# Kernel tuning notes

Measured on AMD Instinct MI355X. Metric: run time of the kernel, lower is better.

Reference implementation:

```python
import jax, jax.numpy as jnp
import numpy as np

B, H, W, C = 2, 64, 64, 320
GROUPS, EPS = 16, 1e-3  # keras GroupNormalization defaults (C>16 -> groups=16)


def quick_gelu(x):
    return x * jax.nn.sigmoid(x * 1.702)


def group_norm(x, gamma, beta):
    b, h, w, c = x.shape
    xg = x.reshape(b, h, w, GROUPS, c // GROUPS)
    mean = xg.mean(axis=(1, 2, 4), keepdims=True)
    var = xg.var(axis=(1, 2, 4), keepdims=True)
    xg = (xg - mean) * jax.lax.rsqrt(var + EPS)
    return xg.reshape(b, h, w, c) * gamma + beta


def attention(q_in, kv_in, wq, bq, wk, bk, wv, bv, wp, bp):
    # q_in, kv_in: [B,H,W,C]
    b, h, w, c = q_in.shape
    n = h * w
    scale = jnp.asarray(c, q_in.dtype) ** -0.5
    q = (q_in @ wq + bq).reshape(b, n, c)
    k = (kv_in @ wk + bk).reshape(b, n, c)
    v = (kv_in @ wv + bv).reshape(b, n, c)
    s = jax.nn.softmax(jnp.einsum('bnc,bmc->bnm', q, k) * scale, axis=-1)  # [B,N,N]
    o = jnp.einsum('bnm,bmc->bnc', s, v).reshape(b, h, w, c)
    return o @ wp + bp


def setup_inputs() -> dict:
    key = jax.random.key(0)
    ks = jax.random.split(key, 16)
    d = {
        'x': jax.random.normal(ks[0], (B, H, W, C), jnp.float32),
        'context': jax.random.normal(ks[1], (B, H, W, C), jnp.float32),
    }
    names = ['sa_q_w', 'sa_k_w', 'sa_v_w', 'sa_p_w', 'ca_q_w', 'ca_k_w', 'ca_v_w', 'ca_p_w']
    for i, nm in enumerate(names):
        d[nm] = jax.random.normal(ks[2 + i], (C, C), jnp.float32) * 0.02
        d[nm.replace('_w', '_b')] = jnp.zeros((C,), jnp.float32)
    d['ca_norm_g'] = jnp.ones((C,), jnp.float32)
    d['ca_norm_b'] = jnp.zeros((C,), jnp.float32)
    d['geglu_w'] = jax.random.normal(ks[10], (C, 8 * C), jnp.float32) * 0.02  # Conv2D 1x1 -> dense
    d['geglu_b'] = jnp.zeros((8 * C,), jnp.float32)
    d['dense_w'] = jax.random.normal(ks[11], (4 * C, C), jnp.float32) * 0.02
    d['dense_b'] = jnp.zeros((C,), jnp.float32)
    return d


def reference(x, context, sa_q_w, sa_q_b, sa_k_w, sa_k_b, sa_v_w, sa_v_b, sa_p_w, sa_p_b,
              ca_q_w, ca_q_b, ca_k_w, ca_k_b, ca_v_w, ca_v_b, ca_p_w, ca_p_b,
              ca_norm_g, ca_norm_b, geglu_w, geglu_b, dense_w, dense_b):
    # attn1: self-attention (note: its norm is defined but unused in the original call())
    a1 = x + attention(x, x, sa_q_w, sa_q_b, sa_k_w, sa_k_b, sa_v_w, sa_v_b, sa_p_w, sa_p_b)
    x = a1 + x
    # attn2: cross-attention; norm applied to query input, residual uses normalized input
    xn = group_norm(x, ca_norm_g, ca_norm_b)
    a2 = xn + attention(xn, context, ca_q_w, ca_q_b, ca_k_w, ca_k_b, ca_v_w, ca_v_b, ca_p_w, ca_p_b)
    x = a2 + x
    # GEGLU FFN (1x1 convs == dense over channels)
    xp = x @ geglu_w + geglu_b  # [B,H,W,8C]
    hdim = 4 * x.shape[-1]
    ff = xp[..., :hdim] * quick_gelu(xp[..., hdim:])
    return ff @ dense_w + dense_b + x
```

## Files before the change

### kernel.cpp

```cpp
#include <hip/hip_runtime.h>
#include <math.h>
#include <stdint.h>


typedef unsigned short u16;
typedef __attribute__((ext_vector_type(8))) short bf16x8;
typedef __attribute__((ext_vector_type(8))) unsigned short u16x8;
typedef __attribute__((ext_vector_type(4))) float f32x4;

constexpr int Bb = 2, Cc = 320;
constexpr int Nn = 64 * 64;
constexpr int Mm = Bb * Nn;
constexpr int GROUPS = 16, CG = Cc / GROUPS;
constexpr float EPS = 1e-3f;
constexpr int GN_SPLIT = 8;
constexpr int KVS = 4;
constexpr int KVC = Nn / KVS;
constexpr int KVT = 32;
constexpr float THR = 8.f;

__device__ __forceinline__ u16 f2b(float f) {
  unsigned u = __float_as_uint(f);
  unsigned r = u + 0x7fffu + ((u >> 16) & 1u);
  return (u16)(r >> 16);
}
__device__ __forceinline__ float b2f(u16 h) {
  return __uint_as_float(((unsigned)h) << 16);
}

template <bool F32OUT, bool DUAL>
__global__ __launch_bounds__(256) void gemm_nt(
    const u16* __restrict__ A, int lda, long long aZ,
    const u16* __restrict__ B, int ldb, long long bZ,
    const float* __restrict__ bias,
    const float* __restrict__ R1, float alpha1,
    const float* __restrict__ R2,
    void* __restrict__ Cp, int ldc, long long cZ,
    u16* __restrict__ C2,
    int K, float scale) {
  const int z = blockIdx.z;
  A += (long long)z * aZ;
  B += (long long)z * bZ;
  const long long coffz = (long long)z * cZ;

  __shared__ __align__(16) u16 As[128][40];
  __shared__ __align__(16) u16 Bs[64][40];

  const int tid = threadIdx.x;
  const int bm = blockIdx.y * 128, bn = blockIdx.x * 64;
  const int lane = tid & 63;
  const int wid = tid >> 6;
  const int wm = (wid >> 1) * 64, wn = (wid & 1) * 32;
  const int lr = lane & 15, lk = (lane >> 4) * 8;

  const int sr = tid >> 2;
  const int sk = (tid & 3) * 8;

  f32x4 acc[4][2] = {};

  const u16* Ap0 = A + (size_t)(bm + sr) * lda + sk;
  const u16* Ap1 = A + (size_t)(bm + 64 + sr) * lda + sk;
  const u16* Bp0 = B + (size_t)(bn + sr) * ldb + sk;

  for (int k0 = 0; k0 < K; k0 += 32) {
    *reinterpret_cast<u16x8*>(&As[sr][sk]) =
        *reinterpret_cast<const u16x8*>(Ap0 + k0);
    *reinterpret_cast<u16x8*>(&As[64 + sr][sk]) =
        *reinterpret_cast<const u16x8*>(Ap1 + k0);
    *reinterpret_cast<u16x8*>(&Bs[sr][sk]) =
        *reinterpret_cast<const u16x8*>(Bp0 + k0);
    __syncthreads();

    bf16x8 af[4], bfr[2];
#pragma unroll
    for (int i = 0; i < 4; ++i)
      af[i] = *reinterpret_cast<const bf16x8*>(&As[wm + i * 16 + lr][lk]);
#pragma unroll
    for (int j = 0; j < 2; ++j)
      bfr[j] = *reinterpret_cast<const bf16x8*>(&Bs[wn + j * 16 + lr][lk]);
#pragma unroll
    for (int i = 0; i < 4; ++i)
#pragma unroll
      for (int j = 0; j < 2; ++j)
        acc[i][j] = __builtin_amdgcn_mfma_f32_16x16x32_bf16(af[i], bfr[j],
                                                            acc[i][j], 0, 0, 0);
    __syncthreads();
  }

  float* Cf = (float*)Cp;
  u16* Cb = (u16*)Cp;
#pragma unroll
  for (int i = 0; i < 4; ++i)
#pragma unroll
    for (int j = 0; j < 2; ++j)
#pragma unroll
      for (int r = 0; r < 4; ++r) {
        const int row = bm + wm + i * 16 + (lane >> 4) * 4 + r;
        const int col = bn + wn + j * 16 + lr;
        const long long off = (long long)row * ldc + col + coffz;
        float v = acc[i][j][r] * scale;
        if (bias) v += bias[col];
        if (R1) v += alpha1 * R1[off];
        if (R2) v += R2[off];
        if (F32OUT) Cf[off] = v; else Cb[off] = f2b(v);
        if (DUAL) C2[off] = f2b(v);
      }
}

__global__ __launch_bounds__(256, 2) void flash_k(
    const u16* __restrict__ qb, const u16* __restrict__ kb,
    const u16* __restrict__ vtb, float* __restrict__ pO,
    float* __restrict__ pml, float scale) {
  const int qt = blockIdx.x, s = blockIdx.y, b = blockIdx.z;
  const int tid = threadIdx.x, wave = tid >> 6, lane = tid & 63;
  const int lr = lane & 15, hi = lane >> 4;
  const int qrow = qt * 64 + wave * 16;

  __shared__ __align__(16) u16 Ks[KVT][336];
  __shared__ __align__(16) u16 Vts[Cc][40];
  __shared__ __align__(16) u16 plds[4][16][40];

  bf16x8 qreg[10];
  const long long qbase = ((long long)b * Nn + qrow + lr) * Cc;
#pragma unroll
  for (int ks = 0; ks < 10; ++ks)
    qreg[ks] = *reinterpret_cast<const bf16x8*>(qb + qbase + ks * 32 + hi * 8);

  f32x4 accO[20] = {};
  float m[4] = {-INFINITY, -INFINITY, -INFINITY, -INFINITY};
  float l[4] = {0.f, 0.f, 0.f, 0.f};

  const u16* kbb = kb + (long long)b * Nn * Cc;
  const u16* vtbb = vtb + (long long)b * Cc * Nn;
  const int kv0 = s * KVC;

  const int krow = tid >> 3;
  const int kcb = tid & 7;
  u16x8 kst[5], vst[5];

  auto issue = [&](int t) {
    const int kvb = kv0 + t * KVT;
#pragma unroll
    for (int c = 0; c < 5; ++c)
      kst[c] = *reinterpret_cast<const u16x8*>(
          kbb + (long long)(kvb + krow) * Cc + (kcb + 8 * c) * 8);
#pragma unroll
    for (int c = 0; c < 5; ++c) {
      const int id = tid + 256 * c;
      const int vr = id >> 2, vc = id & 3;
      vst[c] = *reinterpret_cast<const u16x8*>(
          vtbb + (long long)vr * Nn + kvb + vc * 8);
    }
  };

  issue(0);
  constexpr int NT = KVC / KVT;
  for (int t = 0; t < NT; ++t) {
    __syncthreads();
#pragma unroll
    for (int c = 0; c < 5; ++c)
      *reinterpret_cast<u16x8*>(&Ks[krow][(kcb + 8 * c) * 8]) = kst[c];
#pragma unroll
    for (int c = 0; c < 5; ++c) {
      const int id = tid + 256 * c;
      const int vr = id >> 2, vc = id & 3;
      *reinterpret_cast<u16x8*>(&Vts[vr][vc * 8]) = vst[c];
    }
    __syncthreads();

    if (t + 1 < NT) issue(t + 1);

    f32x4 accS[2] = {};
    __builtin_amdgcn_s_setprio(1);
#pragma unroll
    for (int ks = 0; ks < 10; ++ks) {
#pragma unroll
      for (int j = 0; j < 2; ++j) {
        const bf16x8 bv =
            *reinterpret_cast<const bf16x8*>(&Ks[j * 16 + lr][ks * 32 + hi * 8]);
        accS[j] =
            __builtin_amdgcn_mfma_f32_16x16x32_bf16(qreg[ks], bv, accS[j], 0, 0, 0);
      }
    }
    __builtin_amdgcn_s_setprio(0);

#pragma unroll
    for (int j = 0; j < 2; ++j)
#pragma unroll
      for (int r = 0; r < 4; ++r) accS[j][r] *= scale;

    float tm[4];
#pragma unroll
    for (int r = 0; r < 4; ++r) {
      float tv = fmaxf(accS[0][r], accS[1][r]);
#pragma unroll
      for (int off = 1; off < 16; off <<= 1) tv = fmaxf(tv, __shfl_xor(tv, off, 64));
      tm[r] = tv;
    }
    const bool grow = (tm[0] > m[0] + THR) | (tm[1] > m[1] + THR) |
                      (tm[2] > m[2] + THR) | (tm[3] > m[3] + THR);
    if (__any(grow)) {
      float resc[4];
#pragma unroll
      for (int r = 0; r < 4; ++r) {
        const float mn = fmaxf(m[r], tm[r]);
        resc[r] = __expf(m[r] - mn);
        m[r] = mn;
        l[r] *= resc[r];
      }
#pragma unroll
      for (int n = 0; n < 20; ++n)
#pragma unroll
        for (int r = 0; r < 4; ++r) accO[n][r] *= resc[r];
    }
#pragma unroll
    for (int r = 0; r < 4; ++r) {
      float ps = 0.f;
#pragma unroll
      for (int j = 0; j < 2; ++j) {
        const float p = __expf(accS[j][r] - m[r]);
        accS[j][r] = p;
        ps += p;
      }
#pragma unroll
      for (int off = 1; off < 16; off <<= 1) ps += __shfl_xor(ps, off, 64);
      l[r] += ps;
    }

#pragma unroll
    for (int j = 0; j < 2; ++j)
#pragma unroll
      for (int r = 0; r < 4; ++r)
        plds[wave][hi * 4 + r][j * 16 + lr] = f2b(accS[j][r]);

    {
      const bf16x8 pa = *reinterpret_cast<const bf16x8*>(&plds[wave][lr][hi * 8]);
      __builtin_amdgcn_s_setprio(1);
#pragma unroll
      for (int n = 0; n < 20; ++n) {
        const bf16x8 bv =
            *reinterpret_cast<const bf16x8*>(&Vts[n * 16 + lr][hi * 8]);
        accO[n] = __builtin_amdgcn_mfma_f32_16x16x32_bf16(pa, bv, accO[n], 0, 0, 0);
      }
      __builtin_amdgcn_s_setprio(0);
    }
  }

  const long long obase = (((long long)(s * Bb + b)) * Nn + qrow) * Cc;
#pragma unroll
  for (int n = 0; n < 20; ++n)
#pragma unroll
    for (int r = 0; r < 4; ++r)
      pO[obase + (long long)(hi * 4 + r) * Cc + n * 16 + lr] = accO[n][r];
  if (lr == 0) {
#pragma unroll
    for (int r = 0; r < 4; ++r) {
      const long long mlb =
          (((long long)(s * Bb + b)) * Nn + qrow + hi * 4 + r) * 2;
      pml[mlb] = m[r];
      pml[mlb + 1] = l[r];
    }
  }
}

__global__ __launch_bounds__(256) void fcomb(const float* __restrict__ pO,
                                             const float* __restrict__ pml,
                                             u16* __restrict__ ob) {
  const int row = blockIdx.x * 8 + (threadIdx.x >> 5);
  const int lane32 = threadIdx.x & 31;
  const int b = row >> 12, rb = row & 4095;
  float ms[KVS], ls[KVS], mm = -INFINITY;
#pragma unroll
  for (int s = 0; s < KVS; ++s) {
    const long long i = (((long long)(s * Bb + b)) * Nn + rb) * 2;
    ms[s] = pml[i];
    ls[s] = pml[i + 1];
    mm = fmaxf(mm, ms[s]);
  }
  float w[KVS], den = 0.f;
#pragma unroll
  for (int s = 0; s < KVS; ++s) {
    w[s] = __expf(ms[s] - mm);
    den += w[s] * ls[s];
  }
  const float inv = 1.0f / den;
#pragma unroll
  for (int k = 0; k < 3; ++k) {
    const int c = k * 128 + lane32 * 4;
    if (c < Cc) {
      float4 o = {0.f, 0.f, 0.f, 0.f};
#pragma unroll
      for (int s = 0; s < KVS; ++s) {
        const float4 v = *reinterpret_cast<const float4*>(
            pO + (((long long)(s * Bb + b)) * Nn + rb) * Cc + c);
        o.x += w[s] * v.x;
        o.y += w[s] * v.y;
        o.z += w[s] * v.z;
        o.w += w[s] * v.w;
      }
      ushort4 u;
      u.x = f2b(o.x * inv);
      u.y = f2b(o.y * inv);
      u.z = f2b(o.z * inv);
      u.w = f2b(o.w * inv);
      *reinterpret_cast<ushort4*>(ob + (long long)row * Cc + c) = u;
    }
  }
}

__global__ __launch_bounds__(256) void cast_b(const float* __restrict__ in,
                                              u16* __restrict__ out) {
  const size_t i = ((size_t)blockIdx.x * 256 + threadIdx.x) * 4;
  const float4 v = *reinterpret_cast<const float4*>(in + i);
  ushort4 o;
  o.x = f2b(v.x); o.y = f2b(v.y); o.z = f2b(v.z); o.w = f2b(v.w);
  *reinterpret_cast<ushort4*>(out + i) = o;
}

__global__ __launch_bounds__(256) void tran_f2b(const float* __restrict__ in,
                                                u16* __restrict__ out, int R,
                                                int C, long long inZ,
                                                long long outZ) {
  in += (long long)blockIdx.z * inZ;
  out += (long long)blockIdx.z * outZ;
  __shared__ u16 t[32][33];
  const int c0 = blockIdx.x * 32, r0 = blockIdx.y * 32;
  const int tx = threadIdx.x, ty = threadIdx.y;
#pragma unroll
  for (int i = 0; i < 32; i += 8)
    t[ty + i][tx] = f2b(in[(size_t)(r0 + ty + i) * C + c0 + tx]);
  __syncthreads();
#pragma unroll
  for (int i = 0; i < 32; i += 8)
    out[(size_t)(c0 + ty + i) * R + r0 + tx] = t[tx][ty + i];
}

__global__ __launch_bounds__(256) void gn_stats(const float* __restrict__ x,
                                                float* __restrict__ partials) {
  const int s = blockIdx.x % GN_SPLIT;
  const int bg = blockIdx.x / GN_SPLIT;
  const int b = bg / GROUPS, g = bg % GROUPS;
  const int rows = Nn / GN_SPLIT;
  const float* base = x + (size_t)b * Nn * Cc + g * CG;
  float sum = 0.f, sq = 0.f;
  for (int i = threadIdx.x; i < rows * CG; i += 256) {
    const int r = i / CG, c = i % CG;
    const float v = base[(size_t)(s * rows + r) * Cc + c];
    sum += v; sq += v * v;
  }
#pragma unroll
  for (int off = 32; off >= 1; off >>= 1) {
    sum += __shfl_xor(sum, off, 64);
    sq += __shfl_xor(sq, off, 64);
  }
  __shared__ float rs[4], rq[4];
  const int tid = threadIdx.x;
  if ((tid & 63) == 0) { rs[tid >> 6] = sum; rq[tid >> 6] = sq; }
  __syncthreads();
  if (tid == 0) {
    partials[(bg * GN_SPLIT + s) * 2 + 0] = rs[0] + rs[1] + rs[2] + rs[3];
    partials[(bg * GN_SPLIT + s) * 2 + 1] = rq[0] + rq[1] + rq[2] + rq[3];
  }
}

__global__ __launch_bounds__(256) void gn_apply(
    const float* __restrict__ x, const float* __restrict__ partials,
    const float* __restrict__ gamma, const float* __restrict__ beta,
    float* __restrict__ xn, u16* __restrict__ xnb) {
  const size_t idx = (size_t)blockIdx.x * 256 + threadIdx.x;
  const int c = (int)(idx % Cc);
  const size_t row = idx / Cc;
  const int b = (int)(row / Nn);
  const int bg = b * GROUPS + c / CG;
  float sum = 0.f, sq = 0.f;
#pragma unroll
  for (int s = 0; s < GN_SPLIT; ++s) {
    sum += partials[(bg * GN_SPLIT + s) * 2 + 0];
    sq += partials[(bg * GN_SPLIT + s) * 2 + 1];
  }
  const float cnt = (float)Nn * CG;
  const float mean = sum / cnt;
  const float var = sq / cnt - mean * mean;
  const float r = rsqrtf(var + EPS);
  const float v = (x[idx] - mean) * r * gamma[c] + beta[c];
  xn[idx] = v;
  xnb[idx] = f2b(v);
}

__global__ __launch_bounds__(256) void geglu_comb(const u16* __restrict__ g1,
                                                  const u16* __restrict__ g2,
                                                  u16* __restrict__ ff) {
  const size_t i = ((size_t)blockIdx.x * 256 + threadIdx.x) * 4;
  const ushort4 a = *reinterpret_cast<const ushort4*>(g1 + i);
  const ushort4 b = *reinterpret_cast<const ushort4*>(g2 + i);
  ushort4 o;
  float v1, v2;
  v1 = b2f(a.x); v2 = b2f(b.x);
  o.x = f2b(v1 * (v2 / (1.0f + __expf(-1.702f * v2))));
  v1 = b2f(a.y); v2 = b2f(b.y);
  o.y = f2b(v1 * (v2 / (1.0f + __expf(-1.702f * v2))));
  v1 = b2f(a.z); v2 = b2f(b.z);
  o.z = f2b(v1 * (v2 / (1.0f + __expf(-1.702f * v2))));
  v1 = b2f(a.w); v2 = b2f(b.w);
  o.w = f2b(v1 * (v2 / (1.0f + __expf(-1.702f * v2))));
  *reinterpret_cast<ushort4*>(ff + i) = o;
}

extern "C" void kernel_launch(void* const* d_in, const int* in_sizes, int n_in,
                              void* d_out, int out_size, void* d_ws,
                              size_t ws_size, hipStream_t stream) {
  const float* x   = (const float*)d_in[0];
  const float* ctx = (const float*)d_in[1];
  const float* W[8];
  const float* Bv[8];
  for (int i = 0; i < 8; ++i) {
    W[i]  = (const float*)d_in[2 + 2 * i];
    Bv[i] = (const float*)d_in[3 + 2 * i];
  }
  const float* gn_g = (const float*)d_in[18];
  const float* gn_b = (const float*)d_in[19];
  const float* gw   = (const float*)d_in[20];
  const float* gb   = (const float*)d_in[21];
  const float* dw   = (const float*)d_in[22];
  const float* db   = (const float*)d_in[23];
  float* out = (float*)d_out;

  char* base = (char*)d_ws;
  size_t o = 0;
  auto alloc = [&](size_t bytes) {
    void* p = base + o;
    o = (o + bytes + 255) & ~(size_t)255;
    return p;
  };
  u16* wT[8];
  for (int i = 0; i < 8; ++i) wT[i] = (u16*)alloc(320 * 320 * 2);
  u16* gwT  = (u16*)alloc((size_t)2560 * 320 * 2);
  u16* dwT  = (u16*)alloc((size_t)320 * 1280 * 2);
  u16* xb   = (u16*)alloc((size_t)Mm * Cc * 2);
  u16* ctxb = (u16*)alloc((size_t)Mm * Cc * 2);
  float* x2 = (float*)alloc((size_t)Mm * Cc * 4);
  float* xn = (float*)alloc((size_t)Mm * Cc * 4);
  u16* xnb  = (u16*)alloc((size_t)Mm * Cc * 2);
  float* x3 = (float*)alloc((size_t)Mm * Cc * 4);
  u16* x3b  = (u16*)alloc((size_t)Mm * Cc * 2);
  float* stats = (float*)alloc(4096);
  const size_t SCRSZ = (size_t)20971520 + (size_t)KVS * Bb * Nn * Cc * 4 + 1048576;
  char* SCR = (char*)alloc(SCRSZ);
  u16* qb   = (u16*)SCR;
  u16* kb   = (u16*)(SCR + 5242880);
  u16* vtb  = (u16*)(SCR + 10485760);
  u16* ob   = (u16*)(SCR + 15728640);
  char* REST = SCR + 20971520;
  float* vf  = (float*)REST;
  float* pO  = (float*)REST;
  float* pml = (float*)(REST + (size_t)KVS * Bb * Nn * Cc * 4);
  u16* g1b = (u16*)SCR;
  u16* g2b = (u16*)(SCR + 20971520);
  u16* ffb = (u16*)(SCR + 41943040);

  if (base == nullptr || ws_size < o) return;

  const float scale = 1.0f / sqrtf((float)Cc);
  const long long NC = (long long)Nn * Cc;

  auto gemm_b = [&](const u16* A, int lda, long long aZ, const u16* B, int ldb,
                    long long bZ, const float* bias, u16* C, int ldc,
                    long long cZ, int Mr, int Nc, int K, float sc, int nz) {
    dim3 grid(Nc / 64, Mr / 128, nz);
    gemm_nt<false, false><<<grid, 256, 0, stream>>>(
        A, lda, aZ, B, ldb, bZ, bias, nullptr, 0.f, nullptr, C, ldc, cZ,
        nullptr, K, sc);
  };
  auto gemm_f = [&](const u16* A, int lda, const u16* B, int ldb,
                    const float* bias, const float* R1, float a1,
                    const float* R2, float* C, int ldc, int Mr, int Nc, int K) {
    dim3 grid(Nc / 64, Mr / 128, 1);
    gemm_nt<true, false><<<grid, 256, 0, stream>>>(
        A, lda, 0, B, ldb, 0, bias, R1, a1, R2, C, ldc, 0, nullptr, K, 1.f);
  };

  cast_b<<<(Mm * Cc) / 1024, 256, 0, stream>>>(x, xb);
  cast_b<<<(Mm * Cc) / 1024, 256, 0, stream>>>(ctx, ctxb);
  for (int i = 0; i < 8; ++i)
    tran_f2b<<<dim3(10, 10, 1), dim3(32, 8), 0, stream>>>(W[i], wT[i], 320, 320, 0, 0);
  tran_f2b<<<dim3(80, 10, 1), dim3(32, 8), 0, stream>>>(gw, gwT, 320, 2560, 0, 0);
  tran_f2b<<<dim3(10, 40, 1), dim3(32, 8), 0, stream>>>(dw, dwT, 1280, 320, 0, 0);

  auto attention = [&](const u16* qsrc, const u16* kv, int wi) {
    gemm_b(qsrc, Cc, 0, wT[wi + 0], Cc, 0, Bv[wi + 0], qb, Cc, 0, Mm, Cc, Cc, 1.f, 1);
    gemm_b(kv,   Cc, 0, wT[wi + 1], Cc, 0, Bv[wi + 1], kb, Cc, 0, Mm, Cc, Cc, 1.f, 1);
    {
      dim3 grid(Cc / 64, Mm / 128, 1);
      gemm_nt<true, false><<<grid, 256, 0, stream>>>(
          kv, Cc, 0, wT[wi + 2], Cc, 0, Bv[wi + 2], nullptr, 0.f, nullptr, vf,
          Cc, 0, nullptr, Cc, 1.f);
    }
    tran_f2b<<<dim3(Cc / 32, Nn / 32, 2), dim3(32, 8), 0, stream>>>(
        vf, vtb, Nn, Cc, NC, NC);
    flash_k<<<dim3(Nn / 64, KVS, Bb), 256, 0, stream>>>(qb, kb, vtb, pO, pml,
                                                        scale);
    fcomb<<<Mm / 8, 256, 0, stream>>>(pO, pml, ob);
  };

  attention(xb, xb, 0);
  gemm_f(ob, Cc, wT[3], Cc, Bv[3], x, 2.0f, nullptr, x2, Cc, Mm, Cc, Cc);

  gn_stats<<<Bb * GROUPS * GN_SPLIT, 256, 0, stream>>>(x2, stats);
  gn_apply<<<(Mm * Cc) / 256, 256, 0, stream>>>(x2, stats, gn_g, gn_b, xn, xnb);

  attention(xnb, ctxb, 4);
  {
    dim3 grid(Cc / 64, Mm / 128, 1);
    gemm_nt<true, true><<<grid, 256, 0, stream>>>(
        ob, Cc, 0, wT[7], Cc, 0, Bv[7], xn, 1.0f, x2, x3, Cc, 0, x3b, Cc, 1.f);
  }

  gemm_b(x3b, Cc, 0, gwT, Cc, 0, gb, g1b, 1280, 0, Mm, 1280, Cc, 1.f, 1);
  gemm_b(x3b, Cc, 0, gwT + (size_t)1280 * 320, Cc, 0, gb + 1280, g2b, 1280, 0,
         Mm, 1280, Cc, 1.f, 1);
  geglu_comb<<<(int)(((size_t)Mm * 1280) / 1024), 256, 0, stream>>>(g1b, g2b, ffb);
  gemm_f(ffb, 1280, dwT, 1280, db, x3, 1.0f, nullptr, out, Cc, Mm, Cc, 1280);
}
```

Measured before the change: 607.0 us.

## Fuse QKV projections into one GEMM with transposed V epilogue

Concatenates the Q/K/V (and cross-attention K/V) weights into single wide GEMM launches. V columns are written directly in transposed bf16 layout from the GEMM epilogue, which removes the fp32 V buffer and the separate transpose kernel. It also batches the eight weight transposes into one launch and merges the two GEGLU GEMMs into one 2560-wide GEMM. The cost is strided transposed stores with poor coalescing in the epilogue, plus a bias-concatenation kernel.

```diff
diff --git a/kernel.cpp b/kernel.cpp
--- a/kernel.cpp
+++ b/kernel.cpp
@@ -28,7 +28,7 @@
   return __uint_as_float(((unsigned)h) << 16);
 }
 
-template <bool F32OUT, bool DUAL>
+template <bool F32OUT, bool DUAL, bool VTS>
 __global__ __launch_bounds__(256) void gemm_nt(
     const u16* __restrict__ A, int lda, long long aZ,
     const u16* __restrict__ B, int ldb, long long bZ,
@@ -37,6 +37,7 @@
     const float* __restrict__ R2,
     void* __restrict__ Cp, int ldc, long long cZ,
     u16* __restrict__ C2,
+    u16* __restrict__ VT, int vtc0,
     int K, float scale) {
   const int z = blockIdx.z;
   A += (long long)z * aZ;
@@ -92,23 +93,35 @@
 #pragma unroll
   for (int i = 0; i < 4; ++i)
 #pragma unroll
-    for (int j = 0; j < 2; ++j)
-#pragma unroll
-      for (int r = 0; r < 4; ++r) {
-        const int row = bm + wm + i * 16 + (lane >> 4) * 4 + r;
-        const int col = bn + wn + j * 16 + lr;
-        const long long off = (long long)row * ldc + col + coffz;
-        float v = acc[i][j][r] * scale;
-        if (bias) v += bias[col];
-        if (R1) v += alpha1 * R1[off];
-        if (R2) v += R2[off];
-        if (F32OUT) Cf[off] = v; else Cb[off] = f2b(v);
-        if (DUAL) C2[off] = f2b(v);
+    for (int j = 0; j < 2; ++j) {
+      const int col = bn + wn + j * 16 + lr;
+      const int row0 = bm + wm + i * 16 + (lane >> 4) * 4;
+      if (VTS && col >= vtc0) {
+        const int c = col - vtc0;
+        const int bz = row0 >> 12, rb = row0 & 4095;
+        ushort4 u;
+        u.x = f2b(acc[i][j][0] * scale + bias[col]);
+        u.y = f2b(acc[i][j][1] * scale + bias[col]);
+        u.z = f2b(acc[i][j][2] * scale + bias[col]);
+        u.w = f2b(acc[i][j][3] * scale + bias[col]);
+        *reinterpret_cast<ushort4*>(VT + ((long long)bz * Cc + c) * Nn + rb) = u;
+      } else {
+#pragma unroll
+        for (int r = 0; r < 4; ++r) {
+          const long long off = (long long)(row0 + r) * ldc + col + coffz;
+          float v = acc[i][j][r] * scale;
+          if (bias) v += bias[col];
+          if (R1) v += alpha1 * R1[off];
+          if (R2) v += R2[off];
+          if (F32OUT) Cf[off] = v; else Cb[off] = f2b(v);
+          if (DUAL) C2[off] = f2b(v);
+        }
       }
+    }
 }
 
 __global__ __launch_bounds__(256, 2) void flash_k(
-    const u16* __restrict__ qb, const u16* __restrict__ kb,
+    const u16* __restrict__ q, int qlda, const u16* __restrict__ k, int klda,
     const u16* __restrict__ vtb, float* __restrict__ pO,
     float* __restrict__ pml, float scale) {
   const int qt = blockIdx.x, s = blockIdx.y, b = blockIdx.z;
@@ -121,16 +134,16 @@
   __shared__ __align__(16) u16 plds[4][16][40];
 
   bf16x8 qreg[10];
-  const long long qbase = ((long long)b * Nn + qrow + lr) * Cc;
+  const long long qbase = ((long long)b * Nn + qrow + lr) * qlda;
 #pragma unroll
   for (int ks = 0; ks < 10; ++ks)
-    qreg[ks] = *reinterpret_cast<const bf16x8*>(qb + qbase + ks * 32 + hi * 8);
+    qreg[ks] = *reinterpret_cast<const bf16x8*>(q + qbase + ks * 32 + hi * 8);
 
   f32x4 accO[20] = {};
   float m[4] = {-INFINITY, -INFINITY, -INFINITY, -INFINITY};
   float l[4] = {0.f, 0.f, 0.f, 0.f};
 
-  const u16* kbb = kb + (long long)b * Nn * Cc;
+  const u16* kbb = k + (long long)b * Nn * klda;
   const u16* vtbb = vtb + (long long)b * Cc * Nn;
   const int kv0 = s * KVC;
 
@@ -143,7 +156,7 @@
 #pragma unroll
     for (int c = 0; c < 5; ++c)
       kst[c] = *reinterpret_cast<const u16x8*>(
-          kbb + (long long)(kvb + krow) * Cc + (kcb + 8 * c) * 8);
+          kbb + (long long)(kvb + krow) * klda + (kcb + 8 * c) * 8);
 #pragma unroll
     for (int c = 0; c < 5; ++c) {
       const int id = tid + 256 * c;
@@ -285,8 +298,8 @@
   }
   const float inv = 1.0f / den;
 #pragma unroll
-  for (int k = 0; k < 3; ++k) {
-    const int c = k * 128 + lane32 * 4;
+  for (int kk = 0; kk < 3; ++kk) {
+    const int c = kk * 128 + lane32 * 4;
     if (c < Cc) {
       float4 o = {0.f, 0.f, 0.f, 0.f};
 #pragma unroll
@@ -319,10 +332,7 @@
 
 __global__ __launch_bounds__(256) void tran_f2b(const float* __restrict__ in,
                                                 u16* __restrict__ out, int R,
-                                                int C, long long inZ,
-                                                long long outZ) {
-  in += (long long)blockIdx.z * inZ;
-  out += (long long)blockIdx.z * outZ;
+                                                int C) {
   __shared__ u16 t[32][33];
   const int c0 = blockIdx.x * 32, r0 = blockIdx.y * 32;
   const int tx = threadIdx.x, ty = threadIdx.y;
@@ -333,6 +343,33 @@
 #pragma unroll
   for (int i = 0; i < 32; i += 8)
     out[(size_t)(c0 + ty + i) * R + r0 + tx] = t[tx][ty + i];
+}
+
+struct P8 { const float* p[8]; };
+__global__ __launch_bounds__(256) void tran8(P8 ps, u16* __restrict__ outall) {
+  const float* in = ps.p[blockIdx.z];
+  u16* out = outall + (size_t)blockIdx.z * 320 * 320;
+  __shared__ u16 t[32][33];
+  const int c0 = blockIdx.x * 32, r0 = blockIdx.y * 32;
+  const int tx = threadIdx.x, ty = threadIdx.y;
+#pragma unroll
+  for (int i = 0; i < 32; i += 8)
+    t[ty + i][tx] = f2b(in[(size_t)(r0 + ty + i) * 320 + c0 + tx]);
+  __syncthreads();
+#pragma unroll
+  for (int i = 0; i < 32; i += 8)
+    out[(size_t)(c0 + ty + i) * 320 + r0 + tx] = t[tx][ty + i];
+}
+
+__global__ __launch_bounds__(256) void prep_bias(
+    const float* a, const float* b, const float* c, const float* d,
+    const float* e, float* __restrict__ o) {
+  const int i = blockIdx.x * 256 + threadIdx.x;
+  if (i < 320) o[i] = a[i];
+  else if (i < 640) o[i] = b[i - 320];
+  else if (i < 960) o[i] = c[i - 640];
+  else if (i < 1280) o[i] = d[i - 960];
+  else if (i < 1600) o[i] = e[i - 1280];
 }
 
 __global__ __launch_bounds__(256) void gn_stats(const float* __restrict__ x,
@@ -387,12 +424,13 @@
   xnb[idx] = f2b(v);
 }
 
-__global__ __launch_bounds__(256) void geglu_comb(const u16* __restrict__ g1,
-                                                  const u16* __restrict__ g2,
+__global__ __launch_bounds__(256) void geglu_comb(const u16* __restrict__ xp,
                                                   u16* __restrict__ ff) {
   const size_t i = ((size_t)blockIdx.x * 256 + threadIdx.x) * 4;
-  const ushort4 a = *reinterpret_cast<const ushort4*>(g1 + i);
-  const ushort4 b = *reinterpret_cast<const ushort4*>(g2 + i);
+  const size_t row = i / 1280, c = i % 1280;
+  const u16* p = xp + row * 2560;
+  const ushort4 a = *reinterpret_cast<const ushort4*>(p + c);
+  const ushort4 b = *reinterpret_cast<const ushort4*>(p + 1280 + c);
   ushort4 o;
   float v1, v2;
   v1 = b2f(a.x); v2 = b2f(b.x);
@@ -432,8 +470,7 @@
     o = (o + bytes + 255) & ~(size_t)255;
     return p;
   };
-  u16* wT[8];
-  for (int i = 0; i < 8; ++i) wT[i] = (u16*)alloc(320 * 320 * 2);
+  u16* wTall = (u16*)alloc((size_t)8 * 320 * 320 * 2);
   u16* gwT  = (u16*)alloc((size_t)2560 * 320 * 2);
   u16* dwT  = (u16*)alloc((size_t)320 * 1280 * 2);
   u16* xb   = (u16*)alloc((size_t)Mm * Cc * 2);
@@ -443,81 +480,70 @@
   u16* xnb  = (u16*)alloc((size_t)Mm * Cc * 2);
   float* x3 = (float*)alloc((size_t)Mm * Cc * 4);
   u16* x3b  = (u16*)alloc((size_t)Mm * Cc * 2);
+  float* biasCat = (float*)alloc(1600 * 4);
   float* stats = (float*)alloc(4096);
-  const size_t SCRSZ = (size_t)20971520 + (size_t)KVS * Bb * Nn * Cc * 4 + 1048576;
+  const size_t FIXED = 26214400;
+  const size_t POSZ = (size_t)KVS * Bb * Nn * Cc * 4;
+  const size_t SCRSZ = FIXED + POSZ + 524288;
   char* SCR = (char*)alloc(SCRSZ);
-  u16* qb   = (u16*)SCR;
-  u16* kb   = (u16*)(SCR + 5242880);
-  u16* vtb  = (u16*)(SCR + 10485760);
-  u16* ob   = (u16*)(SCR + 15728640);
-  char* REST = SCR + 20971520;
-  float* vf  = (float*)REST;
+  u16* qkb = (u16*)SCR;
+  u16* kb  = (u16*)(SCR + 10485760);
+  u16* vtb = (u16*)(SCR + 15728640);
+  u16* ob  = (u16*)(SCR + 20971520);
+  char* REST = SCR + FIXED;
   float* pO  = (float*)REST;
-  float* pml = (float*)(REST + (size_t)KVS * Bb * Nn * Cc * 4);
-  u16* g1b = (u16*)SCR;
-  u16* g2b = (u16*)(SCR + 20971520);
-  u16* ffb = (u16*)(SCR + 41943040);
+  float* pml = (float*)(REST + POSZ);
+  u16* xp = (u16*)REST;
+  u16* ffb = (u16*)x2;
 
   if (base == nullptr || ws_size < o) return;
 
   const float scale = 1.0f / sqrtf((float)Cc);
-  const long long NC = (long long)Nn * Cc;
-
-  auto gemm_b = [&](const u16* A, int lda, long long aZ, const u16* B, int ldb,
-                    long long bZ, const float* bias, u16* C, int ldc,
-                    long long cZ, int Mr, int Nc, int K, float sc, int nz) {
-    dim3 grid(Nc / 64, Mr / 128, nz);
-    gemm_nt<false, false><<<grid, 256, 0, stream>>>(
-        A, lda, aZ, B, ldb, bZ, bias, nullptr, 0.f, nullptr, C, ldc, cZ,
-        nullptr, K, sc);
-  };
-  auto gemm_f = [&](const u16* A, int lda, const u16* B, int ldb,
-                    const float* bias, const float* R1, float a1,
-                    const float* R2, float* C, int ldc, int Mr, int Nc, int K) {
-    dim3 grid(Nc / 64, Mr / 128, 1);
-    gemm_nt<true, false><<<grid, 256, 0, stream>>>(
-        A, lda, 0, B, ldb, 0, bias, R1, a1, R2, C, ldc, 0, nullptr, K, 1.f);
-  };
+  u16* wT[8];
+  for (int i = 0; i < 8; ++i) wT[i] = wTall + (size_t)i * 320 * 320;
 
   cast_b<<<(Mm * Cc) / 1024, 256, 0, stream>>>(x, xb);
   cast_b<<<(Mm * Cc) / 1024, 256, 0, stream>>>(ctx, ctxb);
-  for (int i = 0; i < 8; ++i)
-    tran_f2b<<<dim3(10, 10, 1), dim3(32, 8), 0, stream>>>(W[i], wT[i], 320, 320, 0, 0);
-  tran_f2b<<<dim3(80, 10, 1), dim3(32, 8), 0, stream>>>(gw, gwT, 320, 2560, 0, 0);
-  tran_f2b<<<dim3(10, 40, 1), dim3(32, 8), 0, stream>>>(dw, dwT, 1280, 320, 0, 0);
-
-  auto attention = [&](const u16* qsrc, const u16* kv, int wi) {
-    gemm_b(qsrc, Cc, 0, wT[wi + 0], Cc, 0, Bv[wi + 0], qb, Cc, 0, Mm, Cc, Cc, 1.f, 1);
-    gemm_b(kv,   Cc, 0, wT[wi + 1], Cc, 0, Bv[wi + 1], kb, Cc, 0, Mm, Cc, Cc, 1.f, 1);
-    {
-      dim3 grid(Cc / 64, Mm / 128, 1);
-      gemm_nt<true, false><<<grid, 256, 0, stream>>>(
-          kv, Cc, 0, wT[wi + 2], Cc, 0, Bv[wi + 2], nullptr, 0.f, nullptr, vf,
-          Cc, 0, nullptr, Cc, 1.f);
-    }
-    tran_f2b<<<dim3(Cc / 32, Nn / 32, 2), dim3(32, 8), 0, stream>>>(
-        vf, vtb, Nn, Cc, NC, NC);
-    flash_k<<<dim3(Nn / 64, KVS, Bb), 256, 0, stream>>>(qb, kb, vtb, pO, pml,
-                                                        scale);
-    fcomb<<<Mm / 8, 256, 0, stream>>>(pO, pml, ob);
-  };
-
-  attention(xb, xb, 0);
-  gemm_f(ob, Cc, wT[3], Cc, Bv[3], x, 2.0f, nullptr, x2, Cc, Mm, Cc, Cc);
+  {
+    P8 ps;
+    for (int i = 0; i < 8; ++i) ps.p[i] = W[i];
+    tran8<<<dim3(10, 10, 8), dim3(32, 8), 0, stream>>>(ps, wTall);
+  }
+  tran_f2b<<<dim3(80, 10), dim3(32, 8), 0, stream>>>(gw, gwT, 320, 2560);
+  tran_f2b<<<dim3(10, 40), dim3(32, 8), 0, stream>>>(dw, dwT, 1280, 320);
+  prep_bias<<<7, 256, 0, stream>>>(Bv[0], Bv[1], Bv[2], Bv[5], Bv[6], biasCat);
+
+  gemm_nt<false, false, true><<<dim3(15, 64, 1), 256, 0, stream>>>(
+      xb, Cc, 0, wT[0], Cc, 0, biasCat, nullptr, 0.f, nullptr, qkb, 640, 0,
+      nullptr, vtb, 640, Cc, 1.f);
+  flash_k<<<dim3(Nn / 64, KVS, Bb), 256, 0, stream>>>(qkb, 640, qkb + 320, 640,
+                                                      vtb, pO, pml, scale);
+  fcomb<<<Mm / 8, 256, 0, stream>>>(pO, pml, ob);
+  gemm_nt<true, false, false><<<dim3(5, 64, 1), 256, 0, stream>>>(
+      ob, Cc, 0, wT[3], Cc, 0, Bv[3], x, 2.0f, nullptr, x2, Cc, 0, nullptr,
+      nullptr, 0, Cc, 1.f);
 
   gn_stats<<<Bb * GROUPS * GN_SPLIT, 256, 0, stream>>>(x2, stats);
   gn_apply<<<(Mm * Cc) / 256, 256, 0, stream>>>(x2, stats, gn_g, gn_b, xn, xnb);
 
-  attention(xnb, ctxb, 4);
-  {
-    dim3 grid(Cc / 64, Mm / 128, 1);
-    gemm_nt<true, true><<<grid, 256, 0, stream>>>(
-        ob, Cc, 0, wT[7], Cc, 0, Bv[7], xn, 1.0f, x2, x3, Cc, 0, x3b, Cc, 1.f);
-  }
-
-  gemm_b(x3b, Cc, 0, gwT, Cc, 0, gb, g1b, 1280, 0, Mm, 1280, Cc, 1.f, 1);
-  gemm_b(x3b, Cc, 0, gwT + (size_t)1280 * 320, Cc, 0, gb + 1280, g2b, 1280, 0,
-         Mm, 1280, Cc, 1.f, 1);
-  geglu_comb<<<(int)(((size_t)Mm * 1280) / 1024), 256, 0, stream>>>(g1b, g2b, ffb);
-  gemm_f(ffb, 1280, dwT, 1280, db, x3, 1.0f, nullptr, out, Cc, Mm, Cc, 1280);
-}
+  gemm_nt<false, false, false><<<dim3(5, 64, 1), 256, 0, stream>>>(
+      xnb, Cc, 0, wT[4], Cc, 0, Bv[4], nullptr, 0.f, nullptr, qkb, 320, 0,
+      nullptr, nullptr, 0, Cc, 1.f);
+  gemm_nt<false, false, true><<<dim3(10, 64, 1), 256, 0, stream>>>(
+      ctxb, Cc, 0, wT[5], Cc, 0, biasCat + 960, nullptr, 0.f, nullptr, kb, 320,
+      0, nullptr, vtb, 320, Cc, 1.f);
+  flash_k<<<dim3(Nn / 64, KVS, Bb), 256, 0, stream>>>(qkb, 320, kb, 320, vtb,
+                                                      pO, pml, scale);
+  fcomb<<<Mm / 8, 256, 0, stream>>>(pO, pml, ob);
+  gemm_nt<true, true, false><<<dim3(5, 64, 1), 256, 0, stream>>>(
+      ob, Cc, 0, wT[7], Cc, 0, Bv[7], xn, 1.0f, x2, x3, Cc, 0, x3b, nullptr, 0,
+      Cc, 1.f);
+
+  gemm_nt<false, false, false><<<dim3(40, 64, 1), 256, 0, stream>>>(
+      x3b, Cc, 0, gwT, Cc, 0, gb, nullptr, 0.f, nullptr, xp, 2560, 0, nullptr,
+      nullptr, 0, Cc, 1.f);
+  geglu_comb<<<(int)(((size_t)Mm * 1280) / 1024), 256, 0, stream>>>(xp, ffb);
+  gemm_nt<true, false, false><<<dim3(5, 64, 1), 256, 0, stream>>>(
+      ffb, 1280, 0, dwT, 1280, 0, db, x3, 1.0f, nullptr, out, Cc, 0, nullptr,
+      nullptr, 0, 1280, 1.f);
+}
```

After: 551.8 us. -9.1%, faster.
